# Performance work log

Measured on AMD Instinct MI355X. Metric: run time of the kernel, lower is better.

The kernel has to match this reference:

```python
import jax, jax.numpy as jnp
import numpy as np

B, N = 64, 256          # batch, numatoms
ATOMEMB = 20            # hardcoded atomemb_dim
DFEAT = 25              # gaussian centers: arange(0.0, 5.0, 0.2)
MU_MIN, MU_MAX, DELTA_MU, SIGMA = 0.0, 5.0, 0.2, 0.5


def setup_inputs() -> dict:
    key = jax.random.key(0)
    ks = jax.random.split(key, 8)
    s = 0.1
    z = jax.random.randint(ks[0], (B, N), 0, N)
    dist = jax.random.uniform(ks[1], (B, N, N), dtype=jnp.float32) * 5.0
    emb = jax.random.normal(ks[2], (N, ATOMEMB), dtype=jnp.float32) * s
    Vw = jax.random.normal(ks[3], (ATOMEMB, ATOMEMB + DFEAT), dtype=jnp.float32) * s
    Vb = jnp.zeros((ATOMEMB,), dtype=jnp.float32)
    W1 = jax.random.normal(ks[4], (10, ATOMEMB), dtype=jnp.float32) * s
    b1 = jnp.zeros((10,), dtype=jnp.float32)
    W2 = jax.random.normal(ks[5], (1, 10), dtype=jnp.float32) * s
    b2 = jnp.zeros((1,), dtype=jnp.float32)
    return dict(z=z, dist=dist, emb=emb, Vw=Vw, Vb=Vb, W1=W1, b1=b1, W2=W2, b2=b2)


def reference(z, dist, emb, Vw, Vb, W1, b1, W2, b2):
    mask = (z != 0).astype(dist.dtype)                      # [B,N]
    cfeat = emb[z] * mask[..., None]                        # [B,N,20]
    # expand atom features over neighbor axis j and re-apply i-mask (as in source)
    cexp = jnp.broadcast_to(cfeat[:, :, None, :], (B, N, N, ATOMEMB))
    cexp = cexp * mask[:, :, None, None]
    # Gaussian RBF expansion of pairwise distances -> [B,N,N,25]
    mus = jnp.arange(MU_MIN, MU_MAX, DELTA_MU, dtype=dist.dtype)
    dfeat = jnp.exp(-((dist[..., None] - mus) ** 2) / (2.0 * SIGMA ** 2))
    pair = jnp.concatenate([cexp, dfeat], axis=-1)          # [B,N,N,45]
    # message MLP V: Linear(45->20) + Tanh, masked on atom i
    msg = jnp.tanh(jnp.einsum('bijf,of->bijo', pair, Vw) + Vb)
    msg = msg * mask[:, :, None, None]
    agg = msg.sum(axis=2)                                   # sum over neighbors j
    c = cfeat + agg                                         # [B,N,20]
    # top: Tanh -> Linear(20->10) -> Linear(10->1)
    h = jnp.tanh(c) @ W1.T + b1
    e = h @ W2.T + b2                                       # [B,N,1]
    return e.sum(axis=1).squeeze(-1)                        # [B]
```

## Files before the change

kernel.cpp:

```cpp
#include <hip/hip_runtime.h>

#define Bsz 64
#define Nn  256
#define Ee  20
#define Dd  25
#define NBLK 2048

using short8  = __attribute__((ext_vector_type(8))) short;
using floatx4 = __attribute__((ext_vector_type(4))) float;

#if __has_builtin(__builtin_amdgcn_exp2f)
#define EXP2F(x) __builtin_amdgcn_exp2f(x)
#else
#define EXP2F(x) __expf(0.6931471805599453f * (x))
#endif
#if __has_builtin(__builtin_amdgcn_rcpf)
#define RCPF(x) __builtin_amdgcn_rcpf(x)
#else
#define RCPF(x) (1.0f / (x))
#endif

__device__ __forceinline__ short f2bf(float x) {
    unsigned u = __float_as_uint(x);
    unsigned r = (u + 0x7FFFu + ((u >> 16) & 1u)) >> 16;
    return (short)r;
}
__device__ __forceinline__ float bf2f(short h) {
    return __uint_as_float(((unsigned)(unsigned short)h) << 16);
}
__device__ __forceinline__ float tanhfast(float x) {
    float e = __expf(2.0f * x);
    return 1.0f - 2.0f / (e + 1.0f);
}
__device__ __forceinline__ unsigned packbf(float a, float b) {
#if __has_builtin(__builtin_amdgcn_perm)
    return __builtin_amdgcn_perm(__float_as_uint(b) + 0x8000u,
                                 __float_as_uint(a) + 0x8000u, 0x07060302u);
#else
    unsigned ua = (__float_as_uint(a) + 0x8000u) >> 16;
    unsigned ub = (__float_as_uint(b) + 0x8000u) & 0xFFFF0000u;
    return ua | ub;
#endif
}

__global__ __launch_bounds__(256, 4) void dtnn_main(
    const int*   __restrict__ z,
    const float* __restrict__ dist,
    const float* __restrict__ emb,
    const float* __restrict__ Vw,
    const float* __restrict__ Vb,
    const float* __restrict__ W1,
    const float* __restrict__ W2,
    float*       __restrict__ part)
{
    const int tid  = threadIdx.x;
    const int lane = tid & 63;
    const int wave = tid >> 6;
    const int blk  = blockIdx.x;
    const int b    = blk >> 5;
    const int i0   = ((blk & 31) << 3) | (wave << 1);

    const int c16  = lane & 15;
    const int quad = lane >> 4;
    const int k0   = quad * 8;
    const float Kc = 2.8853900817779268f;
    const float T04 = 1.1541560327111707f;

    const float* dr0 = dist + ((size_t)b * Nn + i0) * Nn;
    const float a0r = dr0[lane],        a1r = dr0[lane + 64];
    const float a2r = dr0[lane + 128],  a3r = dr0[lane + 192];
    const float b0r = dr0[Nn + lane],       b1r = dr0[Nn + lane + 64];
    const float b2r = dr0[Nn + lane + 128], b3r = dr0[Nn + lane + 192];

    const int zi0 = z[b * Nn + i0];
    const int zi1 = z[b * Nn + i0 + 1];
    const int zu0 = __builtin_amdgcn_readfirstlane(zi0);
    const int zu1 = __builtin_amdgcn_readfirstlane(zi1);
    const float m0 = (zu0 != 0) ? 1.0f : 0.0f;
    const float m1 = (zu1 != 0) ? 1.0f : 0.0f;

    const float cj[8] = {1.0f, 0.9231163463866358f, 0.7261490370736909f,
                         0.48675225595997157f, 0.2780373004531941f,
                         0.1353352832366127f, 0.05613476283303940f,
                         0.019841459768337877f};

    short8 whiK[2], wloK[2];
    floatx4 bias0[2], bias1[2];
    float cf0[2], cf1[2];
    #pragma unroll
    for (int nt = 0; nt < 2; ++nt) {
        const int o = nt * 16 + c16;
        const bool valid = (o < Ee);
        const int oc = valid ? o : 0;
        #pragma unroll
        for (int jj = 0; jj < 8; ++jj) {
            const int k = k0 + jj;
            const float v = (valid && k < Dd)
                          ? Kc * cj[jj] * Vw[oc * 45 + 20 + k] : 0.0f;
            const short h = f2bf(v);
            whiK[nt][jj] = h;
            wloK[nt][jj] = f2bf(v - bf2f(h));
        }
        float dot0 = 0.0f, dot1 = 0.0f;
        #pragma unroll
        for (int f = 0; f < Ee; ++f) {
            const float w = valid ? Vw[oc * 45 + f] : 0.0f;
            dot0 = fmaf(w, emb[zu0 * Ee + f], dot0);
            dot1 = fmaf(w, emb[zu1 * Ee + f], dot1);
        }
        const float vb = valid ? Vb[oc] : 0.0f;
        const float A0 = Kc * (vb + m0 * dot0);
        const float A1 = Kc * (vb + m1 * dot1);
        bias0[nt] = (floatx4){A0, A0, A0, A0};
        bias1[nt] = (floatx4){A1, A1, A1, A1};
        cf0[nt] = valid ? m0 * emb[zu0 * Ee + oc] : 0.0f;
        cf1[nt] = valid ? m1 * emb[zu1 * Ee + oc] : 0.0f;
    }

    const float mu0 = 0.2f * (float)k0;
    float R00 = 0.0f, R01 = 0.0f, R10 = 0.0f, R11 = 0.0f;

    #pragma unroll 2
    for (int t = 0; t < 16; ++t) {
        const int srcLane = 16 * (t & 3) + c16;
        float s01 = (t & 4) ? a1r : a0r;
        float s23 = (t & 4) ? a3r : a2r;
        const float dv0 = (t & 8) ? s23 : s01;
        const float d0 = __shfl(dv0, srcLane, 64);
        float u01 = (t & 4) ? b1r : b0r;
        float u23 = (t & 4) ? b3r : b2r;
        const float dv1 = (t & 8) ? u23 : u01;
        const float d1 = __shfl(dv1, srcLane, 64);

        short8 gA, gB;
        {
            const float u = d0 - mu0;
            const float g0 = EXP2F((-Kc * u) * u);
            const float tp = EXP2F(T04 * u);
            const float t2 = tp * tp, t3 = t2 * tp, t4 = t2 * t2;
            const float x1 = g0 * tp, x2 = g0 * t2, x3 = g0 * t3, x4 = g0 * t4;
            union { short8 s; unsigned u4[4]; } G;
            G.u4[0] = packbf(g0, x1);
            G.u4[1] = packbf(x2, x3);
            G.u4[2] = packbf(x4, x1 * t4);
            G.u4[3] = packbf(x2 * t4, x3 * t4);
            gA = G.s;
        }
        {
            const float u = d1 - mu0;
            const float g0 = EXP2F((-Kc * u) * u);
            const float tp = EXP2F(T04 * u);
            const float t2 = tp * tp, t3 = t2 * tp, t4 = t2 * t2;
            const float x1 = g0 * tp, x2 = g0 * t2, x3 = g0 * t3, x4 = g0 * t4;
            union { short8 s; unsigned u4[4]; } G;
            G.u4[0] = packbf(g0, x1);
            G.u4[1] = packbf(x2, x3);
            G.u4[2] = packbf(x4, x1 * t4);
            G.u4[3] = packbf(x2 * t4, x3 * t4);
            gB = G.s;
        }

        floatx4 p00 = __builtin_amdgcn_mfma_f32_16x16x32_bf16(gA, whiK[0], bias0[0], 0, 0, 0);
        p00 = __builtin_amdgcn_mfma_f32_16x16x32_bf16(gA, wloK[0], p00, 0, 0, 0);
        floatx4 p01 = __builtin_amdgcn_mfma_f32_16x16x32_bf16(gA, whiK[1], bias0[1], 0, 0, 0);
        p01 = __builtin_amdgcn_mfma_f32_16x16x32_bf16(gA, wloK[1], p01, 0, 0, 0);
        floatx4 p10 = __builtin_amdgcn_mfma_f32_16x16x32_bf16(gB, whiK[0], bias1[0], 0, 0, 0);
        p10 = __builtin_amdgcn_mfma_f32_16x16x32_bf16(gB, wloK[0], p10, 0, 0, 0);
        floatx4 p11 = __builtin_amdgcn_mfma_f32_16x16x32_bf16(gB, whiK[1], bias1[1], 0, 0, 0);
        p11 = __builtin_amdgcn_mfma_f32_16x16x32_bf16(gB, wloK[1], p11, 0, 0, 0);

        {
            const float A0 = EXP2F(p00[0]) + 1.0f, A1 = EXP2F(p00[1]) + 1.0f;
            const float A2 = EXP2F(p00[2]) + 1.0f, A3 = EXP2F(p00[3]) + 1.0f;
            const float q01 = A0 * A1, q23 = A2 * A3;
            R00 = fmaf(fmaf(q01, A2 + A3, q23 * (A0 + A1)), RCPF(q01 * q23), R00);
        }
        {
            const float A0 = EXP2F(p01[0]) + 1.0f, A1 = EXP2F(p01[1]) + 1.0f;
            const float A2 = EXP2F(p01[2]) + 1.0f, A3 = EXP2F(p01[3]) + 1.0f;
            const float q01 = A0 * A1, q23 = A2 * A3;
            R01 = fmaf(fmaf(q01, A2 + A3, q23 * (A0 + A1)), RCPF(q01 * q23), R01);
        }
        {
            const float A0 = EXP2F(p10[0]) + 1.0f, A1 = EXP2F(p10[1]) + 1.0f;
            const float A2 = EXP2F(p10[2]) + 1.0f, A3 = EXP2F(p10[3]) + 1.0f;
            const float q01 = A0 * A1, q23 = A2 * A3;
            R10 = fmaf(fmaf(q01, A2 + A3, q23 * (A0 + A1)), RCPF(q01 * q23), R10);
        }
        {
            const float A0 = EXP2F(p11[0]) + 1.0f, A1 = EXP2F(p11[1]) + 1.0f;
            const float A2 = EXP2F(p11[2]) + 1.0f, A3 = EXP2F(p11[3]) + 1.0f;
            const float q01 = A0 * A1, q23 = A2 * A3;
            R11 = fmaf(fmaf(q01, A2 + A3, q23 * (A0 + A1)), RCPF(q01 * q23), R11);
        }
    }

    R00 += __shfl_xor(R00, 16, 64);  R00 += __shfl_xor(R00, 32, 64);
    R01 += __shfl_xor(R01, 16, 64);  R01 += __shfl_xor(R01, 32, 64);
    R10 += __shfl_xor(R10, 16, 64);  R10 += __shfl_xor(R10, 32, 64);
    R11 += __shfl_xor(R11, 16, 64);  R11 += __shfl_xor(R11, 32, 64);

    float uo[2];
    #pragma unroll
    for (int nt = 0; nt < 2; ++nt) {
        const int o = nt * 16 + c16;
        const bool valid = (o < Ee);
        const int oc = valid ? o : 0;
        float s = 0.0f;
        #pragma unroll
        for (int p = 0; p < 10; ++p)
            s = fmaf(W2[p], W1[p * Ee + oc], s);
        uo[nt] = valid ? s : 0.0f;
    }

    float e = 0.0f;
    e = fmaf(tanhfast(cf0[0] + m0 * (256.0f - 2.0f * R00)), uo[0], e);
    e = fmaf(tanhfast(cf0[1] + m0 * (256.0f - 2.0f * R01)), uo[1], e);
    e = fmaf(tanhfast(cf1[0] + m1 * (256.0f - 2.0f * R10)), uo[0], e);
    e = fmaf(tanhfast(cf1[1] + m1 * (256.0f - 2.0f * R11)), uo[1], e);
    e += __shfl_xor(e, 1, 64);
    e += __shfl_xor(e, 2, 64);
    e += __shfl_xor(e, 4, 64);
    e += __shfl_xor(e, 8, 64);

    __shared__ float sE[4];
    if (lane == 0) sE[wave] = e;
    __syncthreads();
    if (tid == 0)
        part[blk] = sE[0] + sE[1] + sE[2] + sE[3];
}

__global__ __launch_bounds__(64) void dtnn_reduce(
    const float* __restrict__ part,
    const float* __restrict__ b1, const float* __restrict__ W2,
    const float* __restrict__ b2, float* __restrict__ out)
{
    const int b = blockIdx.x;
    const int t = threadIdx.x;
    float v = (t < 32) ? part[b * 32 + t] : 0.0f;
    v += __shfl_xor(v, 1, 64);
    v += __shfl_xor(v, 2, 64);
    v += __shfl_xor(v, 4, 64);
    v += __shfl_xor(v, 8, 64);
    v += __shfl_xor(v, 16, 64);
    if (t == 0) {
        float c0 = b2[0];
        #pragma unroll
        for (int p = 0; p < 10; ++p) c0 = fmaf(W2[p], b1[p], c0);
        out[b] = v + __shfl(v, 32, 64) * 0.0f + 256.0f * c0 + __shfl_xor(v, 32, 64);
    }
}

extern "C" void kernel_launch(void* const* d_in, const int* in_sizes, int n_in,
                              void* d_out, int out_size, void* d_ws, size_t ws_size,
                              hipStream_t stream) {
    const int*   z    = (const int*)  d_in[0];
    const float* dist = (const float*)d_in[1];
    const float* emb  = (const float*)d_in[2];
    const float* Vw   = (const float*)d_in[3];
    const float* Vb   = (const float*)d_in[4];
    const float* W1   = (const float*)d_in[5];
    const float* b1   = (const float*)d_in[6];
    const float* W2   = (const float*)d_in[7];
    const float* b2   = (const float*)d_in[8];
    float* out = (float*)d_out;

    float* partP = (float*)d_ws;

    dtnn_main<<<NBLK, 256, 0, stream>>>(z, dist, emb, Vw, Vb, W1, W2, partP);
    dtnn_reduce<<<Bsz, 64, 0, stream>>>(partP, b1, W2, b2, out);
}
```

Before: 121.9 us.

## Pack tail output columns via DPP and stream dist loads directly

Measured after the change: 120.2 us. No clear change (-1.4%).

```diff
diff --git a/kernel.cpp b/kernel.cpp
--- a/kernel.cpp
+++ b/kernel.cpp
@@ -66,11 +66,7 @@
     const float Kc = 2.8853900817779268f;
     const float T04 = 1.1541560327111707f;
 
-    const float* dr0 = dist + ((size_t)b * Nn + i0) * Nn;
-    const float a0r = dr0[lane],        a1r = dr0[lane + 64];
-    const float a2r = dr0[lane + 128],  a3r = dr0[lane + 192];
-    const float b0r = dr0[Nn + lane],       b1r = dr0[Nn + lane + 64];
-    const float b2r = dr0[Nn + lane + 128], b3r = dr0[Nn + lane + 192];
+    const float* dpl = dist + ((size_t)b * Nn + i0) * Nn + c16;
 
     const int zi0 = z[b * Nn + i0];
     const int zi1 = z[b * Nn + i0 + 1];
@@ -86,7 +82,6 @@
 
     short8 whiK[2], wloK[2];
     floatx4 bias0[2], bias1[2];
-    float cf0[2], cf1[2];
     #pragma unroll
     for (int nt = 0; nt < 2; ++nt) {
         const int o = nt * 16 + c16;
@@ -113,28 +108,25 @@
         const float A1 = Kc * (vb + m1 * dot1);
         bias0[nt] = (floatx4){A0, A0, A0, A0};
         bias1[nt] = (floatx4){A1, A1, A1, A1};
-        cf0[nt] = valid ? m0 * emb[zu0 * Ee + oc] : 0.0f;
-        cf1[nt] = valid ? m1 * emb[zu1 * Ee + oc] : 0.0f;
     }
 
     const float mu0 = 0.2f * (float)k0;
-    float R00 = 0.0f, R01 = 0.0f, R10 = 0.0f, R11 = 0.0f;
+    float Rm0 = 0.0f, Rm1 = 0.0f;
+    float Rt0 = 0.0f, Rt1 = 0.0f;
+
+    float d0 = dpl[0];
+    float d1 = dpl[Nn];
 
     #pragma unroll 2
     for (int t = 0; t < 16; ++t) {
-        const int srcLane = 16 * (t & 3) + c16;
-        float s01 = (t & 4) ? a1r : a0r;
-        float s23 = (t & 4) ? a3r : a2r;
-        const float dv0 = (t & 8) ? s23 : s01;
-        const float d0 = __shfl(dv0, srcLane, 64);
-        float u01 = (t & 4) ? b1r : b0r;
-        float u23 = (t & 4) ? b3r : b2r;
-        const float dv1 = (t & 8) ? u23 : u01;
-        const float d1 = __shfl(dv1, srcLane, 64);
+        const float d0c = d0, d1c = d1;
+        const int tn = (t + 1) & 15;
+        d0 = dpl[16 * tn];
+        d1 = dpl[Nn + 16 * tn];
 
         short8 gA, gB;
         {
-            const float u = d0 - mu0;
+            const float u = d0c - mu0;
             const float g0 = EXP2F((-Kc * u) * u);
             const float tp = EXP2F(T04 * u);
             const float t2 = tp * tp, t3 = t2 * tp, t4 = t2 * t2;
@@ -147,7 +139,7 @@
             gA = G.s;
         }
         {
-            const float u = d1 - mu0;
+            const float u = d1c - mu0;
             const float g0 = EXP2F((-Kc * u) * u);
             const float tp = EXP2F(T04 * u);
             const float t2 = tp * tp, t3 = t2 * tp, t4 = t2 * t2;
@@ -169,55 +161,65 @@
         floatx4 p11 = __builtin_amdgcn_mfma_f32_16x16x32_bf16(gB, whiK[1], bias1[1], 0, 0, 0);
         p11 = __builtin_amdgcn_mfma_f32_16x16x32_bf16(gB, wloK[1], p11, 0, 0, 0);
 
+        int r0 = __float_as_int(p01[0]);
+        r0 = __builtin_amdgcn_update_dpp(r0, __float_as_int(p01[1]), 0x114, 0xF, 0x2, false);
+        r0 = __builtin_amdgcn_update_dpp(r0, __float_as_int(p01[2]), 0x118, 0xF, 0x4, false);
+        r0 = __builtin_amdgcn_update_dpp(r0, __float_as_int(p01[3]), 0x11C, 0xF, 0x8, false);
+        const float At0 = EXP2F(__int_as_float(r0)) + 1.0f;
+
+        int r1 = __float_as_int(p11[0]);
+        r1 = __builtin_amdgcn_update_dpp(r1, __float_as_int(p11[1]), 0x114, 0xF, 0x2, false);
+        r1 = __builtin_amdgcn_update_dpp(r1, __float_as_int(p11[2]), 0x118, 0xF, 0x4, false);
+        r1 = __builtin_amdgcn_update_dpp(r1, __float_as_int(p11[3]), 0x11C, 0xF, 0x8, false);
+        const float At1 = EXP2F(__int_as_float(r1)) + 1.0f;
+
         {
             const float A0 = EXP2F(p00[0]) + 1.0f, A1 = EXP2F(p00[1]) + 1.0f;
             const float A2 = EXP2F(p00[2]) + 1.0f, A3 = EXP2F(p00[3]) + 1.0f;
             const float q01 = A0 * A1, q23 = A2 * A3;
-            R00 = fmaf(fmaf(q01, A2 + A3, q23 * (A0 + A1)), RCPF(q01 * q23), R00);
-        }
-        {
-            const float A0 = EXP2F(p01[0]) + 1.0f, A1 = EXP2F(p01[1]) + 1.0f;
-            const float A2 = EXP2F(p01[2]) + 1.0f, A3 = EXP2F(p01[3]) + 1.0f;
-            const float q01 = A0 * A1, q23 = A2 * A3;
-            R01 = fmaf(fmaf(q01, A2 + A3, q23 * (A0 + A1)), RCPF(q01 * q23), R01);
+            const float n4  = fmaf(q01, A2 + A3, q23 * (A0 + A1));
+            const float d4  = q01 * q23;
+            const float inv = RCPF(d4 * At0);
+            Rm0 = fmaf(n4 * At0, inv, Rm0);
+            Rt0 = fmaf(d4, inv, Rt0);
         }
         {
             const float A0 = EXP2F(p10[0]) + 1.0f, A1 = EXP2F(p10[1]) + 1.0f;
             const float A2 = EXP2F(p10[2]) + 1.0f, A3 = EXP2F(p10[3]) + 1.0f;
             const float q01 = A0 * A1, q23 = A2 * A3;
-            R10 = fmaf(fmaf(q01, A2 + A3, q23 * (A0 + A1)), RCPF(q01 * q23), R10);
-        }
-        {
-            const float A0 = EXP2F(p11[0]) + 1.0f, A1 = EXP2F(p11[1]) + 1.0f;
-            const float A2 = EXP2F(p11[2]) + 1.0f, A3 = EXP2F(p11[3]) + 1.0f;
-            const float q01 = A0 * A1, q23 = A2 * A3;
-            R11 = fmaf(fmaf(q01, A2 + A3, q23 * (A0 + A1)), RCPF(q01 * q23), R11);
-        }
-    }
-
-    R00 += __shfl_xor(R00, 16, 64);  R00 += __shfl_xor(R00, 32, 64);
-    R01 += __shfl_xor(R01, 16, 64);  R01 += __shfl_xor(R01, 32, 64);
-    R10 += __shfl_xor(R10, 16, 64);  R10 += __shfl_xor(R10, 32, 64);
-    R11 += __shfl_xor(R11, 16, 64);  R11 += __shfl_xor(R11, 32, 64);
-
-    float uo[2];
+            const float n4  = fmaf(q01, A2 + A3, q23 * (A0 + A1));
+            const float d4  = q01 * q23;
+            const float inv = RCPF(d4 * At1);
+            Rm1 = fmaf(n4 * At1, inv, Rm1);
+            Rt1 = fmaf(d4, inv, Rt1);
+        }
+    }
+
+    Rm0 += __shfl_xor(Rm0, 16, 64);  Rm0 += __shfl_xor(Rm0, 32, 64);
+    Rm1 += __shfl_xor(Rm1, 16, 64);  Rm1 += __shfl_xor(Rm1, 32, 64);
+    Rt0 += __shfl_xor(Rt0, 4, 64);   Rt0 += __shfl_xor(Rt0, 8, 64);
+    Rt0 += __shfl_xor(Rt0, 16, 64);  Rt0 += __shfl_xor(Rt0, 32, 64);
+    Rt1 += __shfl_xor(Rt1, 4, 64);   Rt1 += __shfl_xor(Rt1, 8, 64);
+    Rt1 += __shfl_xor(Rt1, 16, 64);  Rt1 += __shfl_xor(Rt1, 32, 64);
+
+    const int om = c16;
+    const int ot = 16 + (lane & 3);
+    float uom = 0.0f, uot = 0.0f;
     #pragma unroll
-    for (int nt = 0; nt < 2; ++nt) {
-        const int o = nt * 16 + c16;
-        const bool valid = (o < Ee);
-        const int oc = valid ? o : 0;
-        float s = 0.0f;
-        #pragma unroll
-        for (int p = 0; p < 10; ++p)
-            s = fmaf(W2[p], W1[p * Ee + oc], s);
-        uo[nt] = valid ? s : 0.0f;
-    }
+    for (int p = 0; p < 10; ++p) {
+        uom = fmaf(W2[p], W1[p * Ee + om], uom);
+        uot = fmaf(W2[p], W1[p * Ee + ot], uot);
+    }
+    const float cfm0 = m0 * emb[zu0 * Ee + om];
+    const float cfm1 = m1 * emb[zu1 * Ee + om];
+    const float cft0 = m0 * emb[zu0 * Ee + ot];
+    const float cft1 = m1 * emb[zu1 * Ee + ot];
 
     float e = 0.0f;
-    e = fmaf(tanhfast(cf0[0] + m0 * (256.0f - 2.0f * R00)), uo[0], e);
-    e = fmaf(tanhfast(cf0[1] + m0 * (256.0f - 2.0f * R01)), uo[1], e);
-    e = fmaf(tanhfast(cf1[0] + m1 * (256.0f - 2.0f * R10)), uo[0], e);
-    e = fmaf(tanhfast(cf1[1] + m1 * (256.0f - 2.0f * R11)), uo[1], e);
+    e = fmaf(tanhfast(cfm0 + m0 * (256.0f - 2.0f * Rm0)), uom, e);
+    e = fmaf(tanhfast(cfm1 + m1 * (256.0f - 2.0f * Rm1)), uom, e);
+    e = fmaf(tanhfast(cft0 + m0 * (256.0f - 2.0f * Rt0)), 0.25f * uot, e);
+    e = fmaf(tanhfast(cft1 + m1 * (256.0f - 2.0f * Rt1)), 0.25f * uot, e);
     e += __shfl_xor(e, 1, 64);
     e += __shfl_xor(e, 2, 64);
     e += __shfl_xor(e, 4, 64);
```
